# Kernel tuning notes

Measured on AMD Instinct MI355X. Metric: run time of the kernel, lower is better.

## Reference

```python
import jax, jax.numpy as jnp
import numpy as np

N_NODES = 100000
N_EDGES = 3200000
N_GRAPHS = 512
DIM = 64
NF = 4
BN_EPS = 1e-5

_PARAM_SHAPES = [
    ("c1_w1", (DIM, NF), "randn"), ("c1_b1", (DIM,), "randn"),
    ("c1_g1", (DIM,), "ones"), ("c1_be1", (DIM,), "zeros"),
    ("c1_w2", (DIM, DIM), "randn"), ("c1_b2", (DIM,), "randn"),
    ("bn1_g", (DIM,), "ones"), ("bn1_b", (DIM,), "zeros"),
    ("c2_w1", (DIM, DIM), "randn"), ("c2_b1", (DIM,), "randn"),
    ("c2_g1", (DIM,), "ones"), ("c2_be1", (DIM,), "zeros"),
    ("c2_w2", (DIM, DIM), "randn"), ("c2_b2", (DIM,), "randn"),
    ("bn2_g", (DIM,), "ones"), ("bn2_b", (DIM,), "zeros"),
    ("fc0_w", (DIM, NF), "randn"), ("fc0_b", (DIM,), "randn"),
    ("fc1_w", (DIM, DIM), "randn"), ("fc1_b", (DIM,), "randn"),
    ("fc2_w", (DIM, DIM), "randn"), ("fc2_b", (DIM,), "randn"),
    ("pi_w", (DIM, DIM), "randn"), ("pi_b", (DIM,), "randn"),
    ("vf_w", (DIM, DIM), "randn"), ("vf_b", (DIM,), "randn"),
]


def setup_inputs() -> dict:
    key = jax.random.key(0)
    ks = jax.random.split(key, 3 + len(_PARAM_SHAPES))
    inp = {
        "x": jax.random.normal(ks[0], (N_NODES, NF), jnp.float32),
        "edge_index": jax.random.randint(ks[1], (2, N_EDGES), 0, N_NODES, dtype=jnp.int64)
        if jax.config.jax_enable_x64 else jax.random.randint(ks[1], (2, N_EDGES), 0, N_NODES).astype(jnp.int32),
        "batch": jnp.sort(jax.random.randint(ks[2], (N_NODES,), 0, N_GRAPHS)).astype(jnp.int32),
    }
    for i, (name, shape, fill) in enumerate(_PARAM_SHAPES):
        k = ks[3 + i]
        if fill == "randn":
            inp[name] = jax.random.normal(k, shape, jnp.float32) * 0.1
        elif fill == "ones":
            inp[name] = jnp.ones(shape, jnp.float32)
        else:
            inp[name] = jnp.zeros(shape, jnp.float32)
    return inp


def _lin(x, w, b):
    return x @ w.T + b


def _bn(x, g, b):  # training-mode batch statistics over node axis
    m = x.mean(axis=0)
    v = x.var(axis=0)
    return (x - m) * jax.lax.rsqrt(v + BN_EPS) * g + b


def _gin_conv(x, src, dst, w1, b1, g1, be1, w2, b2):
    # sum-aggregate neighbor messages (GINConv, eps=0): h = MLP(x + sum_{j in N(i)} x_j)
    agg = jax.ops.segment_sum(x[src], dst, num_segments=x.shape[0])
    h = x + agg
    h = jax.nn.relu(_bn(_lin(h, w1, b1), g1, be1))
    return _lin(h, w2, b2)


def reference(x, edge_index, batch,
              c1_w1, c1_b1, c1_g1, c1_be1, c1_w2, c1_b2, bn1_g, bn1_b,
              c2_w1, c2_b1, c2_g1, c2_be1, c2_w2, c2_b2, bn2_g, bn2_b,
              fc0_w, fc0_b, fc1_w, fc1_b, fc2_w, fc2_b,
              pi_w, pi_b, vf_w, vf_b):
    src, dst = edge_index[0], edge_index[1]
    h1 = jax.nn.relu(_bn(_gin_conv(x, src, dst, c1_w1, c1_b1, c1_g1, c1_be1, c1_w2, c1_b2), bn1_g, bn1_b))
    h2 = jax.nn.relu(_bn(_gin_conv(h1, src, dst, c2_w1, c2_b1, c2_g1, c2_be1, c2_w2, c2_b2), bn2_g, bn2_b))
    pool = lambda h: jax.ops.segment_sum(h, batch, num_segments=N_GRAPHS)  # global_add_pool
    # dropout is eval-mode identity
    out = _lin(pool(x), fc0_w, fc0_b) + _lin(pool(h1), fc1_w, fc1_b) + _lin(pool(h2), fc2_w, fc2_b)
    pi = jax.nn.relu(_lin(out, pi_w, pi_b))
    vf = jax.nn.relu(_lin(out, vf_w, vf_b))
    return (pi, vf)
```

## Files before the change

### kernel.cpp

```cpp
#include <hip/hip_runtime.h>

#define N_NODES 100000
#define N_EDGES 3200000
#define N_GRAPHS 512
#define NBKT 782
#define NBLK 256
#define EPB 12500
#define NSCAN 200192
#define NB_SCAN 782
#define SCAP 6000

__device__ __forceinline__ uint32_t f2bf(float f) {
  uint32_t u = __float_as_uint(f);
  return (u + 0x7fffu + ((u >> 16) & 1u)) >> 16;
}
__device__ __forceinline__ float bflo(uint32_t u) { return __uint_as_float(u << 16); }
__device__ __forceinline__ float bfhi(uint32_t u) { return __uint_as_float(u & 0xffff0000u); }

__global__ __launch_bounds__(256) void k_cnt(const int* __restrict__ dst,
                                             int* __restrict__ cnt)
{
  __shared__ int h[NBKT];
  int t = threadIdx.x, blk = blockIdx.x;
  for (int i = t; i < NBKT; i += 256) h[i] = 0;
  __syncthreads();
  int e0 = blk * EPB;
  for (int i = t; i < EPB; i += 256) atomicAdd(&h[dst[e0 + i] >> 7], 1);
  __syncthreads();
  for (int i = t; i < NBKT; i += 256) cnt[i * NBLK + blk] = h[i];
}

__global__ __launch_bounds__(256) void k_scan1(const int* __restrict__ v,
                                               int* __restrict__ bsum, int n)
{
  __shared__ int s[256];
  int i = blockIdx.x * 256 + threadIdx.x;
  s[threadIdx.x] = i < n ? v[i] : 0;
  __syncthreads();
  for (int off = 128; off > 0; off >>= 1) {
    if (threadIdx.x < off) s[threadIdx.x] += s[threadIdx.x + off];
    __syncthreads();
  }
  if (threadIdx.x == 0) bsum[blockIdx.x] = s[0];
}

__global__ void k_scan2(int* __restrict__ bsum, int nb)
{
  __shared__ int s[1024];
  int t = threadIdx.x;
  int v = t < nb ? bsum[t] : 0;
  s[t] = v;
  __syncthreads();
  for (int off = 1; off < 1024; off <<= 1) {
    int nv = t >= off ? s[t - off] : 0;
    __syncthreads();
    s[t] += nv;
    __syncthreads();
  }
  if (t < nb) bsum[t] = s[t] - v;
}

__global__ __launch_bounds__(256) void k_scanout(const int* __restrict__ v,
    const int* __restrict__ boff, int* __restrict__ out, int n)
{
  __shared__ int s[256];
  int t = threadIdx.x, i = blockIdx.x * 256 + t;
  int x = i < n ? v[i] : 0;
  s[t] = x;
  __syncthreads();
  for (int off = 1; off < 256; off <<= 1) {
    int nv = t >= off ? s[t - off] : 0;
    __syncthreads();
    s[t] += nv;
    __syncthreads();
  }
  if (i < n) out[i] = boff[blockIdx.x] + s[t] - x;
}

__global__ __launch_bounds__(256) void k_bin(const int* __restrict__ src,
    const int* __restrict__ dst, const int* __restrict__ off,
    int2* __restrict__ eb)
{
  __shared__ int base[NBKT];
  __shared__ int cur[NBKT];
  int t = threadIdx.x, blk = blockIdx.x;
  for (int i = t; i < NBKT; i += 256) { base[i] = off[i * NBLK + blk]; cur[i] = 0; }
  __syncthreads();
  int e0 = blk * EPB;
  for (int i = t; i < EPB; i += 256) {
    int e = e0 + i;
    int s = src[e], d = dst[e], b = d >> 7;
    int p = atomicAdd(&cur[b], 1);
    eb[base[b] + p] = make_int2(s, d);
  }
}

__global__ __launch_bounds__(256) void k_sortb(const int2* __restrict__ eb,
    const int* __restrict__ off, int* __restrict__ rowstart,
    int* __restrict__ csr)
{
  int b = blockIdx.x, t = threadIdx.x;
  int start = off[b * NBLK];
  int end = (b == NBKT - 1) ? N_EDGES : off[(b + 1) * NBLK];
  int cnt = end - start;
  __shared__ int2 ebs[SCAP];
  __shared__ int h[128], cur[128];
  bool staged = cnt <= SCAP;
  if (staged) for (int i = t; i < cnt; i += 256) ebs[i] = eb[start + i];
  if (t < 128) h[t] = 0;
  __syncthreads();
  if (staged) {
    for (int i = t; i < cnt; i += 256) atomicAdd(&h[ebs[i].y & 127], 1);
  } else {
    for (int i = t; i < cnt; i += 256) atomicAdd(&h[eb[start + i].y & 127], 1);
  }
  __syncthreads();
  int v = t < 128 ? h[t] : 0;
  for (int o = 1; o < 128; o <<= 1) {
    int nv = (t < 128 && t >= o) ? h[t - o] : 0;
    __syncthreads();
    if (t < 128) h[t] += nv;
    __syncthreads();
  }
  if (t < 128) {
    int ex = h[t] - v;
    int node = b * 128 + t;
    if (node < N_NODES) rowstart[node] = start + ex;
    cur[t] = ex;
  }
  if (b == NBKT - 1 && t == 0) rowstart[N_NODES] = N_EDGES;
  __syncthreads();
  if (staged) {
    for (int i = t; i < cnt; i += 256) {
      int2 e = ebs[i];
      int p = atomicAdd(&cur[e.y & 127], 1);
      csr[start + p] = e.x;
    }
  } else {
    for (int i = t; i < cnt; i += 256) {
      int2 e = eb[start + i];
      int p = atomicAdd(&cur[e.y & 127], 1);
      csr[start + p] = e.x;
    }
  }
}

__global__ __launch_bounds__(256) void k_gstart(const int* __restrict__ batch,
                                                int* __restrict__ gstart, int n)
{
  int i = blockIdx.x * 256 + threadIdx.x;
  if (i >= n) return;
  int b = batch[i];
  if (i == 0) {
    for (int g = 0; g <= b; ++g) gstart[g] = 0;
  } else {
    int p = batch[i - 1];
    for (int g = p + 1; g <= b; ++g) gstart[g] = i;
  }
  if (i == n - 1) {
    for (int g = b + 1; g <= N_GRAPHS; ++g) gstart[g] = n;
  }
}

__global__ __launch_bounds__(256) void k_agglin1(const int* __restrict__ csr,
    const int* __restrict__ rowstart, const float* __restrict__ x,
    const float* __restrict__ w1, const float* __restrict__ b1,
    float* __restrict__ OUT, float* __restrict__ st, int n)
{
  __shared__ float sAgg[64][4];
  __shared__ float rs[4][64], rq[4][64];
  int t = threadIdx.x;
  int l = t >> 2, f = t & 3;
  int nd = blockIdx.x * 64 + l;
  float acc = 0.f;
  if (nd < n) {
    int e = rowstart[nd], e1 = rowstart[nd + 1];
    for (; e + 4 <= e1; e += 4) {
      int s0 = csr[e], s1 = csr[e + 1], s2 = csr[e + 2], s3 = csr[e + 3];
      acc += x[s0 * 4 + f] + x[s1 * 4 + f] + x[s2 * 4 + f] + x[s3 * 4 + f];
    }
    for (; e < e1; ++e) acc += x[csr[e] * 4 + f];
    acc += x[nd * 4 + f];
  }
  sAgg[l][f] = acc;
  __syncthreads();
  int d = t & 63, slot = t >> 6;
  float4 wr = reinterpret_cast<const float4*>(w1)[d];
  float bv = b1[d];
  float lsum = 0.f, lsq = 0.f;
  int base = blockIdx.x * 64;
  for (int li = slot; li < 64; li += 4) {
    int nn = base + li;
    if (nn >= n) break;
    float v = bv + sAgg[li][0] * wr.x + sAgg[li][1] * wr.y
                 + sAgg[li][2] * wr.z + sAgg[li][3] * wr.w;
    OUT[nn * 64 + d] = v;
    lsum += v; lsq += v * v;
  }
  rs[slot][d] = lsum; rq[slot][d] = lsq;
  __syncthreads();
  if (t < 64) {
    atomicAdd(&st[d],      rs[0][d] + rs[1][d] + rs[2][d] + rs[3][d]);
    atomicAdd(&st[64 + d], rq[0][d] + rq[1][d] + rq[2][d] + rq[3][d]);
  }
}

template <bool WRITE_HB>
__global__ __launch_bounds__(256) void k_hpool(const float* __restrict__ T,
    const float* __restrict__ st, const float* __restrict__ gam,
    const float* __restrict__ bet, float invN, const int* __restrict__ batch,
    uint2* __restrict__ Hb, float* __restrict__ pool)
{
  __shared__ float sm[16][64];
  __shared__ int sb[16];
  __shared__ float s_ss[128];
  int t = threadIdx.x;
  int r = t >> 4, c4 = t & 15;
  int row0 = blockIdx.x * 16;
  if (t < 64) {
    float mean = st[t] * invN;
    float var  = st[64 + t] * invN - mean * mean;
    float sc   = gam[t] * rsqrtf(var + 1e-5f);
    s_ss[t] = sc;
    s_ss[64 + t] = bet[t] - mean * sc;
  }
  if (t >= 64 && t < 80) sb[t - 64] = batch[row0 + t - 64];
  __syncthreads();
  float4 v = reinterpret_cast<const float4*>(T)[(row0 + r) * 16 + c4];
  int c = c4 * 4;
  v.x = fmaxf(v.x * s_ss[c + 0] + s_ss[64 + c + 0], 0.f);
  v.y = fmaxf(v.y * s_ss[c + 1] + s_ss[64 + c + 1], 0.f);
  v.z = fmaxf(v.z * s_ss[c + 2] + s_ss[64 + c + 2], 0.f);
  v.w = fmaxf(v.w * s_ss[c + 3] + s_ss[64 + c + 3], 0.f);
  if (WRITE_HB) {
    uint2 p;
    p.x = f2bf(v.x) | (f2bf(v.y) << 16);
    p.y = f2bf(v.z) | (f2bf(v.w) << 16);
    Hb[(row0 + r) * 16 + c4] = p;
  }
  *reinterpret_cast<float4*>(&sm[r][c]) = v;
  __syncthreads();
  if (t < 64) {
    int gmin = sb[0], gmax = sb[15];
    for (int g = gmin; g <= gmax; ++g) {
      float s = 0.f;
#pragma unroll
      for (int rr = 0; rr < 16; ++rr) if (sb[rr] == g) s += sm[rr][t];
      atomicAdd(&pool[g * 64 + t], s);
    }
  }
}

__global__ __launch_bounds__(256) void k_agg64b(const int* __restrict__ csr,
    const int* __restrict__ rowstart, const uint32_t* __restrict__ Hb,
    float2* __restrict__ AGG, int n)
{
  int hw = threadIdx.x >> 5, lane = threadIdx.x & 31;
  int nd = blockIdx.x * 8 + hw;
  if (nd >= n) return;
  int e = rowstart[nd], e1 = rowstart[nd + 1];
  float a0 = 0.f, a1 = 0.f;
  for (; e + 4 <= e1; e += 4) {
    int s0 = csr[e], s1 = csr[e + 1], s2 = csr[e + 2], s3 = csr[e + 3];
    uint32_t u0 = Hb[s0 * 32 + lane];
    uint32_t u1 = Hb[s1 * 32 + lane];
    uint32_t u2 = Hb[s2 * 32 + lane];
    uint32_t u3 = Hb[s3 * 32 + lane];
    a0 += bflo(u0) + bflo(u1) + bflo(u2) + bflo(u3);
    a1 += bfhi(u0) + bfhi(u1) + bfhi(u2) + bfhi(u3);
  }
  for (; e < e1; ++e) {
    uint32_t u = Hb[csr[e] * 32 + lane];
    a0 += bflo(u); a1 += bfhi(u);
  }
  AGG[nd * 32 + lane] = make_float2(a0, a1);
}

__global__ __launch_bounds__(64) void k_pool_x(const float* __restrict__ x,
    const int* __restrict__ gstart, float* __restrict__ px)
{
  int g = blockIdx.x;
  int r0 = gstart[g], r1 = gstart[g + 1];
  int f = threadIdx.x & 3, slot = threadIdx.x >> 2;
  float acc = 0.f;
  for (int r = r0 + slot; r < r1; r += 16) acc += x[r * 4 + f];
  __shared__ float red[16][4];
  red[slot][f] = acc;
  __syncthreads();
  if (threadIdx.x < 4) {
    float s = 0.f;
    for (int k = 0; k < 16; ++k) s += red[k][f];
    px[g * 4 + f] = s;
  }
}

template <int MODE>
__global__ __launch_bounds__(256) void k_gemm64(const void* __restrict__ IN1,
    const float* __restrict__ IN2, const float* __restrict__ stIn,
    const float* __restrict__ gam, const float* __restrict__ bet, float invN,
    const float* __restrict__ W, const float* __restrict__ bias,
    float* __restrict__ OUT, float* __restrict__ st, int n)
{
  __shared__ float sWt[64][64];
  __shared__ float sIn[16][68];
  __shared__ float s_ss[128];
  __shared__ float rs[4][64], rq[4][64];
  int tid = threadIdx.x;
  for (int i = tid; i < 4096; i += 256) {
    int dd = i >> 6, kk = i & 63;
    sWt[kk][dd ^ kk] = W[i];
  }
  if (MODE == 0 && tid < 64) {
    float mean = stIn[tid] * invN;
    float var  = stIn[64 + tid] * invN - mean * mean;
    float sc   = gam[tid] * rsqrtf(var + 1e-5f);
    s_ss[tid] = sc;
    s_ss[64 + tid] = bet[tid] - mean * sc;
  }
  int d = tid & 63;
  int wav = tid >> 6;
  int srow = tid >> 4, sc4 = tid & 15;
  float bv = bias[d];
  float lsum = 0.f, lsq = 0.f;
  int ngroups = (n + 15) >> 4;
  for (int grp = blockIdx.x; grp < ngroups; grp += gridDim.x) {
    int nbase = grp * 16;
    __syncthreads();
    {
      int nn = nbase + srow;
      float4 v = make_float4(0.f, 0.f, 0.f, 0.f);
      if (nn < n) {
        if (MODE == 0) {
          float4 t = reinterpret_cast<const float4*>(IN2)[nn * 16 + sc4];
          int c = sc4 * 4;
          v.x = fmaxf(t.x * s_ss[c + 0] + s_ss[64 + c + 0], 0.f);
          v.y = fmaxf(t.y * s_ss[c + 1] + s_ss[64 + c + 1], 0.f);
          v.z = fmaxf(t.z * s_ss[c + 2] + s_ss[64 + c + 2], 0.f);
          v.w = fmaxf(t.w * s_ss[c + 3] + s_ss[64 + c + 3], 0.f);
        } else {
          uint2 hb = reinterpret_cast<const uint2*>(IN1)[nn * 16 + sc4];
          float4 b = reinterpret_cast<const float4*>(IN2)[nn * 16 + sc4];
          v.x = bflo(hb.x) + b.x;
          v.y = bfhi(hb.x) + b.y;
          v.z = bflo(hb.y) + b.z;
          v.w = bfhi(hb.y) + b.w;
        }
      }
      *reinterpret_cast<float4*>(&sIn[srow][sc4 * 4]) = v;
    }
    __syncthreads();
    float acc[4];
#pragma unroll
    for (int i = 0; i < 4; i++) acc[i] = bv;
#pragma unroll 4
    for (int k4 = 0; k4 < 16; k4++) {
      float4 rv[4];
#pragma unroll
      for (int i = 0; i < 4; i++)
        rv[i] = *reinterpret_cast<const float4*>(&sIn[wav * 4 + i][k4 * 4]);
#pragma unroll
      for (int j = 0; j < 4; j++) {
        int kk = k4 * 4 + j;
        float wv = sWt[kk][d ^ kk];
#pragma unroll
        for (int i = 0; i < 4; i++) acc[i] += (&rv[i].x)[j] * wv;
      }
    }
#pragma unroll
    for (int i = 0; i < 4; i++) {
      int nn = nbase + wav * 4 + i;
      if (nn < n) {
        OUT[nn * 64 + d] = acc[i];
        lsum += acc[i]; lsq += acc[i] * acc[i];
      }
    }
  }
  __syncthreads();
  rs[wav][d] = lsum; rq[wav][d] = lsq;
  __syncthreads();
  if (tid < 64) {
    atomicAdd(&st[d],      rs[0][d] + rs[1][d] + rs[2][d] + rs[3][d]);
    atomicAdd(&st[64 + d], rq[0][d] + rq[1][d] + rq[2][d] + rq[3][d]);
  }
}

__global__ __launch_bounds__(64) void k_head(const float* __restrict__ px,
    const float* __restrict__ ph1, const float* __restrict__ ph2,
    const float* __restrict__ fc0w, const float* __restrict__ fc0b,
    const float* __restrict__ fc1w, const float* __restrict__ fc1b,
    const float* __restrict__ fc2w, const float* __restrict__ fc2b,
    const float* __restrict__ piw, const float* __restrict__ pib,
    const float* __restrict__ vfw, const float* __restrict__ vfb,
    float* __restrict__ out)
{
  int g = blockIdx.x, d = threadIdx.x;
  float o = fc0b[d] + fc1b[d] + fc2b[d];
  float4 pxv = reinterpret_cast<const float4*>(px)[g];
  float4 w0 = reinterpret_cast<const float4*>(fc0w)[d];
  o += pxv.x * w0.x + pxv.y * w0.y + pxv.z * w0.z + pxv.w * w0.w;
  const float4* p1 = reinterpret_cast<const float4*>(ph1) + g * 16;
  const float4* w1 = reinterpret_cast<const float4*>(fc1w) + d * 16;
  const float4* p2 = reinterpret_cast<const float4*>(ph2) + g * 16;
  const float4* w2 = reinterpret_cast<const float4*>(fc2w) + d * 16;
#pragma unroll
  for (int k = 0; k < 16; k++) {
    float4 a = p1[k], b = w1[k];
    o += a.x * b.x + a.y * b.y + a.z * b.z + a.w * b.w;
    float4 c = p2[k], e = w2[k];
    o += c.x * e.x + c.y * e.y + c.z * e.z + c.w * e.w;
  }
  __shared__ float so[64];
  so[d] = o;
  __syncthreads();
  float p = pib[d], v = vfb[d];
  const float4* sov = reinterpret_cast<const float4*>(so);
  const float4* wp = reinterpret_cast<const float4*>(piw) + d * 16;
  const float4* wv = reinterpret_cast<const float4*>(vfw) + d * 16;
#pragma unroll
  for (int k = 0; k < 16; k++) {
    float4 a = sov[k], b = wp[k], c = wv[k];
    p += a.x * b.x + a.y * b.y + a.z * b.z + a.w * b.w;
    v += a.x * c.x + a.y * c.y + a.z * c.z + a.w * c.w;
  }
  out[g * 64 + d] = fmaxf(p, 0.f);
  out[N_GRAPHS * 64 + g * 64 + d] = fmaxf(v, 0.f);
}

extern "C" void kernel_launch(void* const* d_in, const int* in_sizes, int n_in,
                              void* d_out, int out_size, void* d_ws, size_t ws_size,
                              hipStream_t stream)
{
  const float* x     = (const float*)d_in[0];
  const int*   ei    = (const int*)d_in[1];
  const int*   batch = (const int*)d_in[2];
  const float* c1_w1 = (const float*)d_in[3];
  const float* c1_b1 = (const float*)d_in[4];
  const float* c1_g1 = (const float*)d_in[5];
  const float* c1_be1= (const float*)d_in[6];
  const float* c1_w2 = (const float*)d_in[7];
  const float* c1_b2 = (const float*)d_in[8];
  const float* bn1_g = (const float*)d_in[9];
  const float* bn1_b = (const float*)d_in[10];
  const float* c2_w1 = (const float*)d_in[11];
  const float* c2_b1 = (const float*)d_in[12];
  const float* c2_g1 = (const float*)d_in[13];
  const float* c2_be1= (const float*)d_in[14];
  const float* c2_w2 = (const float*)d_in[15];
  const float* c2_b2 = (const float*)d_in[16];
  const float* bn2_g = (const float*)d_in[17];
  const float* bn2_b = (const float*)d_in[18];
  const float* fc0_w = (const float*)d_in[19];
  const float* fc0_b = (const float*)d_in[20];
  const float* fc1_w = (const float*)d_in[21];
  const float* fc1_b = (const float*)d_in[22];
  const float* fc2_w = (const float*)d_in[23];
  const float* fc2_b = (const float*)d_in[24];
  const float* pi_w  = (const float*)d_in[25];
  const float* pi_b  = (const float*)d_in[26];
  const float* vf_w  = (const float*)d_in[27];
  const float* vf_b  = (const float*)d_in[28];
  const int* src = ei;
  const int* dst = ei + N_EDGES;

  float* ws = (float*)d_ws;
  float* stats    = ws;
  float* ph1      = ws + 512;
  float* ph2      = ws + 33280;
  float* px       = ws + 66560;
  int*   gstart   = (int*)(ws + 68608);
  int*   bsum     = (int*)(ws + 69124);
  int*   rowstart = (int*)(ws + 70160);
  float* U        = ws + 170176;
  int*   cnt      = (int*)U;
  int*   off      = (int*)U + 200192;
  uint32_t* Hb    = (uint32_t*)U;
  int*   csr      = (int*)(ws + 3370176);
  float* A        = ws + 6570176;
  int2*  eb       = (int2*)A;

  const float invN = 1.0f / (float)N_NODES;

  hipMemsetAsync(ws, 0, 66048 * sizeof(float), stream);

  k_cnt    <<<NBLK, 256, 0, stream>>>(dst, cnt);
  k_scan1  <<<NB_SCAN, 256, 0, stream>>>(cnt, bsum, NSCAN);
  k_scan2  <<<1, 1024, 0, stream>>>(bsum, NB_SCAN);
  k_scanout<<<NB_SCAN, 256, 0, stream>>>(cnt, bsum, off, NSCAN);
  k_bin    <<<NBLK, 256, 0, stream>>>(src, dst, off, eb);
  k_sortb  <<<NBKT, 256, 0, stream>>>(eb, off, rowstart, csr);
  k_gstart <<<(N_NODES + 255) / 256, 256, 0, stream>>>(batch, gstart, N_NODES);

  k_pool_x<<<N_GRAPHS, 64, 0, stream>>>(x, gstart, px);

  k_agglin1<<<(N_NODES + 63) / 64, 256, 0, stream>>>(csr, rowstart, x, c1_w1, c1_b1,
                                                     A, stats + 0, N_NODES);
  k_gemm64<0><<<1024, 256, 0, stream>>>(nullptr, A, stats + 0, c1_g1, c1_be1, invN,
                                        c1_w2, c1_b2, A, stats + 128, N_NODES);
  k_hpool<true><<<N_NODES / 16, 256, 0, stream>>>(A, stats + 128, bn1_g, bn1_b, invN,
                                                  batch, (uint2*)Hb, ph1);

  k_agg64b<<<(N_NODES + 7) / 8, 256, 0, stream>>>(csr, rowstart, Hb, (float2*)A, N_NODES);
  k_gemm64<2><<<1024, 256, 0, stream>>>(Hb, A, nullptr, nullptr, nullptr, 0.f,
                                        c2_w1, c2_b1, A, stats + 256, N_NODES);
  k_gemm64<0><<<1024, 256, 0, stream>>>(nullptr, A, stats + 256, c2_g1, c2_be1, invN,
                                        c2_w2, c2_b2, A, stats + 384, N_NODES);
  k_hpool<false><<<N_NODES / 16, 256, 0, stream>>>(A, stats + 384, bn2_g, bn2_b, invN,
                                                   batch, nullptr, ph2);

  k_head<<<N_GRAPHS, 64, 0, stream>>>(px, ph1, ph2, fc0_w, fc0_b, fc1_w, fc1_b,
                                      fc2_w, fc2_b, pi_w, pi_b, vf_w, vf_b, (float*)d_out);
}
```

Baseline: 390.3 us.

## Split bf16 node features into column chunks to shrink gather working set

Stores the layer-1 bf16 activations and the layer-2 intermediates in a chunked (column-block-major) layout. Aggregation then runs as four passes, each gathering one 16-column chunk, so each pass's random-gather working set is a quarter of the full matrix and fits better in cache. The GEMM kernels are rewritten to read inputs straight from global memory in the chunked layout, with no shared-memory staging, and to write chunked outputs. The price is four aggregation launches that each reread the CSR, plus less coalesced direct loads in the GEMM. The GEMM also drops its tail guards (n>>4) and relies on N being a multiple of 16.

```diff
diff --git a/kernel.cpp b/kernel.cpp
--- a/kernel.cpp
+++ b/kernel.cpp
@@ -9,6 +9,8 @@
 #define NSCAN 200192
 #define NB_SCAN 782
 #define SCAP 6000
+#define CH4 (N_NODES * 4)
+#define CH1 (N_NODES * 16)
 
 __device__ __forceinline__ uint32_t f2bf(float f) {
   uint32_t u = __float_as_uint(f);
@@ -205,7 +207,7 @@
   }
 }
 
-template <bool WRITE_HB>
+template <bool WRITE_HB, bool INCH>
 __global__ __launch_bounds__(256) void k_hpool(const float* __restrict__ T,
     const float* __restrict__ st, const float* __restrict__ gam,
     const float* __restrict__ bet, float invN, const int* __restrict__ batch,
@@ -226,7 +228,9 @@
   }
   if (t >= 64 && t < 80) sb[t - 64] = batch[row0 + t - 64];
   __syncthreads();
-  float4 v = reinterpret_cast<const float4*>(T)[(row0 + r) * 16 + c4];
+  int a4 = INCH ? ((c4 >> 2) * CH4 + (row0 + r) * 4 + (c4 & 3))
+                : ((row0 + r) * 16 + c4);
+  float4 v = reinterpret_cast<const float4*>(T)[a4];
   int c = c4 * 4;
   v.x = fmaxf(v.x * s_ss[c + 0] + s_ss[64 + c + 0], 0.f);
   v.y = fmaxf(v.y * s_ss[c + 1] + s_ss[64 + c + 1], 0.f);
@@ -236,7 +240,7 @@
     uint2 p;
     p.x = f2bf(v.x) | (f2bf(v.y) << 16);
     p.y = f2bf(v.z) | (f2bf(v.w) << 16);
-    Hb[(row0 + r) * 16 + c4] = p;
+    Hb[(c4 >> 2) * CH4 + (row0 + r) * 4 + (c4 & 3)] = p;
   }
   *reinterpret_cast<float4*>(&sm[r][c]) = v;
   __syncthreads();
@@ -251,29 +255,27 @@
   }
 }
 
-__global__ __launch_bounds__(256) void k_agg64b(const int* __restrict__ csr,
-    const int* __restrict__ rowstart, const uint32_t* __restrict__ Hb,
-    float2* __restrict__ AGG, int n)
-{
-  int hw = threadIdx.x >> 5, lane = threadIdx.x & 31;
-  int nd = blockIdx.x * 8 + hw;
+__global__ __launch_bounds__(256) void k_agg16(const int* __restrict__ csr,
+    const int* __restrict__ rowstart, const uint32_t* __restrict__ Hbc,
+    float2* __restrict__ AGGc, int n)
+{
+  int wv = threadIdx.x >> 6, lane = threadIdx.x & 63;
+  int esub = lane >> 3, col = lane & 7;
+  int nd = blockIdx.x * 4 + wv;
   if (nd >= n) return;
-  int e = rowstart[nd], e1 = rowstart[nd + 1];
+  int e0 = rowstart[nd], e1 = rowstart[nd + 1];
   float a0 = 0.f, a1 = 0.f;
-  for (; e + 4 <= e1; e += 4) {
-    int s0 = csr[e], s1 = csr[e + 1], s2 = csr[e + 2], s3 = csr[e + 3];
-    uint32_t u0 = Hb[s0 * 32 + lane];
-    uint32_t u1 = Hb[s1 * 32 + lane];
-    uint32_t u2 = Hb[s2 * 32 + lane];
-    uint32_t u3 = Hb[s3 * 32 + lane];
-    a0 += bflo(u0) + bflo(u1) + bflo(u2) + bflo(u3);
-    a1 += bfhi(u0) + bfhi(u1) + bfhi(u2) + bfhi(u3);
-  }
-  for (; e < e1; ++e) {
-    uint32_t u = Hb[csr[e] * 32 + lane];
-    a0 += bflo(u); a1 += bfhi(u);
-  }
-  AGG[nd * 32 + lane] = make_float2(a0, a1);
+  for (int base = e0; base < e1; base += 8) {
+    int e = base + esub;
+    if (e < e1) {
+      uint32_t u = Hbc[csr[e] * 8 + col];
+      a0 += bflo(u); a1 += bfhi(u);
+    }
+  }
+  a0 += __shfl_xor(a0, 8);  a1 += __shfl_xor(a1, 8);
+  a0 += __shfl_xor(a0, 16); a1 += __shfl_xor(a1, 16);
+  a0 += __shfl_xor(a0, 32); a1 += __shfl_xor(a1, 32);
+  if (esub == 0) AGGc[nd * 8 + col] = make_float2(a0, a1);
 }
 
 __global__ __launch_bounds__(64) void k_pool_x(const float* __restrict__ x,
@@ -294,22 +296,18 @@
   }
 }
 
-template <int MODE>
-__global__ __launch_bounds__(256) void k_gemm64(const void* __restrict__ IN1,
+template <int MODE, bool INCH, bool OUTCH>
+__global__ __launch_bounds__(256) void k_gemm64(const uint2* __restrict__ IN1,
     const float* __restrict__ IN2, const float* __restrict__ stIn,
     const float* __restrict__ gam, const float* __restrict__ bet, float invN,
     const float* __restrict__ W, const float* __restrict__ bias,
     float* __restrict__ OUT, float* __restrict__ st, int n)
 {
-  __shared__ float sWt[64][64];
-  __shared__ float sIn[16][68];
+  __shared__ float sWtT[64][68];
   __shared__ float s_ss[128];
   __shared__ float rs[4][64], rq[4][64];
   int tid = threadIdx.x;
-  for (int i = tid; i < 4096; i += 256) {
-    int dd = i >> 6, kk = i & 63;
-    sWt[kk][dd ^ kk] = W[i];
-  }
+  for (int i = tid; i < 4096; i += 256) sWtT[i >> 6][i & 63] = W[i];
   if (MODE == 0 && tid < 64) {
     float mean = stIn[tid] * invN;
     float var  = stIn[64 + tid] * invN - mean * mean;
@@ -317,62 +315,53 @@
     s_ss[tid] = sc;
     s_ss[64 + tid] = bet[tid] - mean * sc;
   }
-  int d = tid & 63;
-  int wav = tid >> 6;
-  int srow = tid >> 4, sc4 = tid & 15;
+  __syncthreads();
+  int d = tid & 63, wav = tid >> 6;
   float bv = bias[d];
   float lsum = 0.f, lsq = 0.f;
-  int ngroups = (n + 15) >> 4;
+  const float4* in2_4 = reinterpret_cast<const float4*>(IN2);
+  const float4* ssc4 = reinterpret_cast<const float4*>(s_ss);
+  const float4* ssh4 = reinterpret_cast<const float4*>(s_ss + 64);
+  int ngroups = n >> 4;
   for (int grp = blockIdx.x; grp < ngroups; grp += gridDim.x) {
-    int nbase = grp * 16;
-    __syncthreads();
-    {
-      int nn = nbase + srow;
-      float4 v = make_float4(0.f, 0.f, 0.f, 0.f);
-      if (nn < n) {
+    int r0 = grp * 16 + wav * 4;
+    float acc[4];
+#pragma unroll
+    for (int i = 0; i < 4; i++) acc[i] = bv;
+#pragma unroll 2
+    for (int k4 = 0; k4 < 16; k4++) {
+      float4 wf = *reinterpret_cast<const float4*>(&sWtT[d][k4 * 4]);
+      float4 rv[4];
+#pragma unroll
+      for (int i = 0; i < 4; i++) {
+        int rr = r0 + i;
+        int a4 = INCH ? ((k4 >> 2) * CH4 + rr * 4 + (k4 & 3)) : (rr * 16 + k4);
         if (MODE == 0) {
-          float4 t = reinterpret_cast<const float4*>(IN2)[nn * 16 + sc4];
-          int c = sc4 * 4;
-          v.x = fmaxf(t.x * s_ss[c + 0] + s_ss[64 + c + 0], 0.f);
-          v.y = fmaxf(t.y * s_ss[c + 1] + s_ss[64 + c + 1], 0.f);
-          v.z = fmaxf(t.z * s_ss[c + 2] + s_ss[64 + c + 2], 0.f);
-          v.w = fmaxf(t.w * s_ss[c + 3] + s_ss[64 + c + 3], 0.f);
+          float4 tt = in2_4[a4];
+          float4 sc = ssc4[k4], sh = ssh4[k4];
+          rv[i].x = fmaxf(tt.x * sc.x + sh.x, 0.f);
+          rv[i].y = fmaxf(tt.y * sc.y + sh.y, 0.f);
+          rv[i].z = fmaxf(tt.z * sc.z + sh.z, 0.f);
+          rv[i].w = fmaxf(tt.w * sc.w + sh.w, 0.f);
         } else {
-          uint2 hb = reinterpret_cast<const uint2*>(IN1)[nn * 16 + sc4];
-          float4 b = reinterpret_cast<const float4*>(IN2)[nn * 16 + sc4];
-          v.x = bflo(hb.x) + b.x;
-          v.y = bfhi(hb.x) + b.y;
-          v.z = bflo(hb.y) + b.z;
-          v.w = bfhi(hb.y) + b.w;
+          uint2 hb = IN1[a4];
+          float4 b = in2_4[a4];
+          rv[i].x = bflo(hb.x) + b.x;
+          rv[i].y = bfhi(hb.x) + b.y;
+          rv[i].z = bflo(hb.y) + b.z;
+          rv[i].w = bfhi(hb.y) + b.w;
         }
       }
-      *reinterpret_cast<float4*>(&sIn[srow][sc4 * 4]) = v;
-    }
-    __syncthreads();
-    float acc[4];
-#pragma unroll
-    for (int i = 0; i < 4; i++) acc[i] = bv;
-#pragma unroll 4
-    for (int k4 = 0; k4 < 16; k4++) {
-      float4 rv[4];
 #pragma unroll
       for (int i = 0; i < 4; i++)
-        rv[i] = *reinterpret_cast<const float4*>(&sIn[wav * 4 + i][k4 * 4]);
-#pragma unroll
-      for (int j = 0; j < 4; j++) {
-        int kk = k4 * 4 + j;
-        float wv = sWt[kk][d ^ kk];
-#pragma unroll
-        for (int i = 0; i < 4; i++) acc[i] += (&rv[i].x)[j] * wv;
-      }
+        acc[i] += rv[i].x * wf.x + rv[i].y * wf.y + rv[i].z * wf.z + rv[i].w * wf.w;
     }
 #pragma unroll
     for (int i = 0; i < 4; i++) {
-      int nn = nbase + wav * 4 + i;
-      if (nn < n) {
-        OUT[nn * 64 + d] = acc[i];
-        lsum += acc[i]; lsq += acc[i] * acc[i];
-      }
+      int rr = r0 + i;
+      int ea = OUTCH ? ((d >> 4) * CH1 + rr * 16 + (d & 15)) : (rr * 64 + d);
+      OUT[ea] = acc[i];
+      lsum += acc[i]; lsq += acc[i] * acc[i];
     }
   }
   __syncthreads();
@@ -494,18 +483,20 @@
 
   k_agglin1<<<(N_NODES + 63) / 64, 256, 0, stream>>>(csr, rowstart, x, c1_w1, c1_b1,
                                                      A, stats + 0, N_NODES);
-  k_gemm64<0><<<1024, 256, 0, stream>>>(nullptr, A, stats + 0, c1_g1, c1_be1, invN,
-                                        c1_w2, c1_b2, A, stats + 128, N_NODES);
-  k_hpool<true><<<N_NODES / 16, 256, 0, stream>>>(A, stats + 128, bn1_g, bn1_b, invN,
-                                                  batch, (uint2*)Hb, ph1);
-
-  k_agg64b<<<(N_NODES + 7) / 8, 256, 0, stream>>>(csr, rowstart, Hb, (float2*)A, N_NODES);
-  k_gemm64<2><<<1024, 256, 0, stream>>>(Hb, A, nullptr, nullptr, nullptr, 0.f,
-                                        c2_w1, c2_b1, A, stats + 256, N_NODES);
-  k_gemm64<0><<<1024, 256, 0, stream>>>(nullptr, A, stats + 256, c2_g1, c2_be1, invN,
-                                        c2_w2, c2_b2, A, stats + 384, N_NODES);
-  k_hpool<false><<<N_NODES / 16, 256, 0, stream>>>(A, stats + 384, bn2_g, bn2_b, invN,
-                                                   batch, nullptr, ph2);
+  k_gemm64<0, false, false><<<1024, 256, 0, stream>>>(nullptr, A, stats + 0,
+      c1_g1, c1_be1, invN, c1_w2, c1_b2, A, stats + 128, N_NODES);
+  k_hpool<true, false><<<N_NODES / 16, 256, 0, stream>>>(A, stats + 128, bn1_g, bn1_b,
+      invN, batch, (uint2*)Hb, ph1);
+
+  for (int c = 0; c < 4; ++c)
+    k_agg16<<<(N_NODES + 3) / 4, 256, 0, stream>>>(csr, rowstart,
+        Hb + (size_t)c * N_NODES * 8, (float2*)A + (size_t)c * N_NODES * 8, N_NODES);
+  k_gemm64<2, true, true><<<1024, 256, 0, stream>>>((const uint2*)Hb, A, nullptr,
+      nullptr, nullptr, 0.f, c2_w1, c2_b1, A, stats + 256, N_NODES);
+  k_gemm64<0, true, true><<<1024, 256, 0, stream>>>(nullptr, A, stats + 256,
+      c2_g1, c2_be1, invN, c2_w2, c2_b2, A, stats + 384, N_NODES);
+  k_hpool<false, true><<<N_NODES / 16, 256, 0, stream>>>(A, stats + 384, bn2_g, bn2_b,
+      invN, batch, nullptr, ph2);
 
   k_head<<<N_GRAPHS, 64, 0, stream>>>(px, ph1, ph2, fc0_w, fc0_b, fc1_w, fc1_b,
                                       fc2_w, fc2_b, pi_w, pi_b, vf_w, vf_b, (float*)d_out);
```

Result: slower. 648.3 us (+66.1%).

## Split bf16 feature table into column chunks and aggregate one chunk per launch

Applied to the files above, without the earlier changes.

The bf16 node-feature table is stored as four column chunks of 16 features each, and the layer-2 neighbor aggregation runs as four separate launches, one per chunk. Each chunk is about 6.4 MB, so it may stay resident in cache while 3.2M random gathers hit it. Each wavefront handles one node, with 8 edges in parallel and 8 columns per edge, and combines partial sums with shuffles. The price is reading the CSR four times, writing the aggregate in chunked layout, and a separate output buffer B for the following GEMMs.

```diff
diff --git a/kernel.cpp b/kernel.cpp
--- a/kernel.cpp
+++ b/kernel.cpp
@@ -9,6 +9,8 @@
 #define NSCAN 200192
 #define NB_SCAN 782
 #define SCAP 6000
+#define CH4 (N_NODES * 4)
+#define CH1 (N_NODES * 16)
 
 __device__ __forceinline__ uint32_t f2bf(float f) {
   uint32_t u = __float_as_uint(f);
@@ -236,7 +238,7 @@
     uint2 p;
     p.x = f2bf(v.x) | (f2bf(v.y) << 16);
     p.y = f2bf(v.z) | (f2bf(v.w) << 16);
-    Hb[(row0 + r) * 16 + c4] = p;
+    Hb[(c4 >> 2) * CH4 + (row0 + r) * 4 + (c4 & 3)] = p;
   }
   *reinterpret_cast<float4*>(&sm[r][c]) = v;
   __syncthreads();
@@ -251,29 +253,27 @@
   }
 }
 
-__global__ __launch_bounds__(256) void k_agg64b(const int* __restrict__ csr,
-    const int* __restrict__ rowstart, const uint32_t* __restrict__ Hb,
-    float2* __restrict__ AGG, int n)
-{
-  int hw = threadIdx.x >> 5, lane = threadIdx.x & 31;
-  int nd = blockIdx.x * 8 + hw;
+__global__ __launch_bounds__(256) void k_agg16(const int* __restrict__ csr,
+    const int* __restrict__ rowstart, const uint32_t* __restrict__ Hbc,
+    float2* __restrict__ AGGc, int n)
+{
+  int wv = threadIdx.x >> 6, lane = threadIdx.x & 63;
+  int esub = lane >> 3, col = lane & 7;
+  int nd = blockIdx.x * 4 + wv;
   if (nd >= n) return;
-  int e = rowstart[nd], e1 = rowstart[nd + 1];
+  int e0 = rowstart[nd], e1 = rowstart[nd + 1];
   float a0 = 0.f, a1 = 0.f;
-  for (; e + 4 <= e1; e += 4) {
-    int s0 = csr[e], s1 = csr[e + 1], s2 = csr[e + 2], s3 = csr[e + 3];
-    uint32_t u0 = Hb[s0 * 32 + lane];
-    uint32_t u1 = Hb[s1 * 32 + lane];
-    uint32_t u2 = Hb[s2 * 32 + lane];
-    uint32_t u3 = Hb[s3 * 32 + lane];
-    a0 += bflo(u0) + bflo(u1) + bflo(u2) + bflo(u3);
-    a1 += bfhi(u0) + bfhi(u1) + bfhi(u2) + bfhi(u3);
-  }
-  for (; e < e1; ++e) {
-    uint32_t u = Hb[csr[e] * 32 + lane];
-    a0 += bflo(u); a1 += bfhi(u);
-  }
-  AGG[nd * 32 + lane] = make_float2(a0, a1);
+  for (int base = e0; base < e1; base += 8) {
+    int e = base + esub;
+    if (e < e1) {
+      uint32_t u = Hbc[csr[e] * 8 + col];
+      a0 += bflo(u); a1 += bfhi(u);
+    }
+  }
+  a0 += __shfl_xor(a0, 8);  a1 += __shfl_xor(a1, 8);
+  a0 += __shfl_xor(a0, 16); a1 += __shfl_xor(a1, 16);
+  a0 += __shfl_xor(a0, 32); a1 += __shfl_xor(a1, 32);
+  if (esub == 0) AGGc[nd * 8 + col] = make_float2(a0, a1);
 }
 
 __global__ __launch_bounds__(64) void k_pool_x(const float* __restrict__ x,
@@ -294,7 +294,7 @@
   }
 }
 
-template <int MODE>
+template <int MODE, bool INCH>
 __global__ __launch_bounds__(256) void k_gemm64(const void* __restrict__ IN1,
     const float* __restrict__ IN2, const float* __restrict__ stIn,
     const float* __restrict__ gam, const float* __restrict__ bet, float invN,
@@ -320,8 +320,8 @@
   int d = tid & 63;
   int wav = tid >> 6;
   int srow = tid >> 4, sc4 = tid & 15;
+  float lsum = 0.f, lsq = 0.f;
   float bv = bias[d];
-  float lsum = 0.f, lsq = 0.f;
   int ngroups = (n + 15) >> 4;
   for (int grp = blockIdx.x; grp < ngroups; grp += gridDim.x) {
     int nbase = grp * 16;
@@ -330,16 +330,17 @@
       int nn = nbase + srow;
       float4 v = make_float4(0.f, 0.f, 0.f, 0.f);
       if (nn < n) {
+        int a4 = INCH ? ((sc4 >> 2) * CH4 + nn * 4 + (sc4 & 3)) : (nn * 16 + sc4);
         if (MODE == 0) {
-          float4 t = reinterpret_cast<const float4*>(IN2)[nn * 16 + sc4];
+          float4 t = reinterpret_cast<const float4*>(IN2)[a4];
           int c = sc4 * 4;
           v.x = fmaxf(t.x * s_ss[c + 0] + s_ss[64 + c + 0], 0.f);
           v.y = fmaxf(t.y * s_ss[c + 1] + s_ss[64 + c + 1], 0.f);
           v.z = fmaxf(t.z * s_ss[c + 2] + s_ss[64 + c + 2], 0.f);
           v.w = fmaxf(t.w * s_ss[c + 3] + s_ss[64 + c + 3], 0.f);
         } else {
-          uint2 hb = reinterpret_cast<const uint2*>(IN1)[nn * 16 + sc4];
-          float4 b = reinterpret_cast<const float4*>(IN2)[nn * 16 + sc4];
+          uint2 hb = reinterpret_cast<const uint2*>(IN1)[a4];
+          float4 b = reinterpret_cast<const float4*>(IN2)[a4];
           v.x = bflo(hb.x) + b.x;
           v.y = bfhi(hb.x) + b.y;
           v.z = bflo(hb.y) + b.z;
@@ -476,6 +477,7 @@
   uint32_t* Hb    = (uint32_t*)U;
   int*   csr      = (int*)(ws + 3370176);
   float* A        = ws + 6570176;
+  float* B        = ws + 12970176;
   int2*  eb       = (int2*)A;
 
   const float invN = 1.0f / (float)N_NODES;
@@ -494,18 +496,20 @@
 
   k_agglin1<<<(N_NODES + 63) / 64, 256, 0, stream>>>(csr, rowstart, x, c1_w1, c1_b1,
                                                      A, stats + 0, N_NODES);
-  k_gemm64<0><<<1024, 256, 0, stream>>>(nullptr, A, stats + 0, c1_g1, c1_be1, invN,
-                                        c1_w2, c1_b2, A, stats + 128, N_NODES);
-  k_hpool<true><<<N_NODES / 16, 256, 0, stream>>>(A, stats + 128, bn1_g, bn1_b, invN,
-                                                  batch, (uint2*)Hb, ph1);
-
-  k_agg64b<<<(N_NODES + 7) / 8, 256, 0, stream>>>(csr, rowstart, Hb, (float2*)A, N_NODES);
-  k_gemm64<2><<<1024, 256, 0, stream>>>(Hb, A, nullptr, nullptr, nullptr, 0.f,
-                                        c2_w1, c2_b1, A, stats + 256, N_NODES);
-  k_gemm64<0><<<1024, 256, 0, stream>>>(nullptr, A, stats + 256, c2_g1, c2_be1, invN,
-                                        c2_w2, c2_b2, A, stats + 384, N_NODES);
-  k_hpool<false><<<N_NODES / 16, 256, 0, stream>>>(A, stats + 384, bn2_g, bn2_b, invN,
-                                                   batch, nullptr, ph2);
+  k_gemm64<0, false><<<1024, 256, 0, stream>>>(nullptr, A, stats + 0,
+      c1_g1, c1_be1, invN, c1_w2, c1_b2, A, stats + 128, N_NODES);
+  k_hpool<true><<<N_NODES / 16, 256, 0, stream>>>(A, stats + 128, bn1_g, bn1_b,
+      invN, batch, (uint2*)Hb, ph1);
+
+  for (int c = 0; c < 4; ++c)
+    k_agg16<<<(N_NODES + 3) / 4, 256, 0, stream>>>(csr, rowstart,
+        Hb + (size_t)c * N_NODES * 8, (float2*)A + (size_t)c * N_NODES * 8, N_NODES);
+  k_gemm64<2, true><<<1024, 256, 0, stream>>>(Hb, A, nullptr,
+      nullptr, nullptr, 0.f, c2_w1, c2_b1, B, stats + 256, N_NODES);
+  k_gemm64<0, false><<<1024, 256, 0, stream>>>(nullptr, B, stats + 256,
+      c2_g1, c2_be1, invN, c2_w2, c2_b2, B, stats + 384, N_NODES);
+  k_hpool<false><<<N_NODES / 16, 256, 0, stream>>>(B, stats + 384, bn2_g, bn2_b,
+      invN, batch, nullptr, ph2);
 
   k_head<<<N_GRAPHS, 64, 0, stream>>>(px, ph1, ph2, fc0_w, fc0_b, fc1_w, fc1_b,
                                       fc2_w, fc2_b, pi_w, pi_b, vf_w, vf_b, (float*)d_out);
```

Result: slower. 503.2 us (+28.9%).
